# Optimization experiments

Measured on AMD Instinct MI355X. Metric: run time of the kernel, lower is better.

## Reference

```python
import jax, jax.numpy as jnp
import numpy as np

N = 100000
E = 1200000
D_IN, D_HID, D_OUT = 64, 64, 32


def setup_inputs() -> dict:
    key = jax.random.key(0)
    ks = jax.random.split(key, 8)
    x = jax.random.normal(ks[0], (N, D_IN), dtype=jnp.float32)
    edge_index = jax.random.randint(ks[1], (2, E), 0, N, dtype=jnp.int64)
    s_in = 1.0 / np.sqrt(D_IN)
    s_hid = 1.0 / np.sqrt(D_HID)
    return {
        "x": x,
        "edge_index": edge_index,
        "W1_l": jax.random.normal(ks[2], (D_IN, D_HID), dtype=jnp.float32) * s_in,
        "W1_r": jax.random.normal(ks[3], (D_IN, D_HID), dtype=jnp.float32) * s_in,
        "b1": jnp.zeros((D_HID,), dtype=jnp.float32),
        "W2_l": jax.random.normal(ks[4], (D_HID, D_OUT), dtype=jnp.float32) * s_hid,
        "W2_r": jax.random.normal(ks[5], (D_HID, D_OUT), dtype=jnp.float32) * s_hid,
        "b2": jnp.zeros((D_OUT,), dtype=jnp.float32),
    }


def _sage_conv(h, src, dst, W_l, W_r, b, n_nodes):
    # mean aggregation of source features onto destination nodes
    summed = jax.ops.segment_sum(h[src], dst, num_segments=n_nodes)  # [N, d]
    deg = jax.ops.segment_sum(jnp.ones((src.shape[0],), h.dtype), dst,
                              num_segments=n_nodes)  # [N]
    mean = summed / jnp.maximum(deg, 1.0)[:, None]
    # PyG SAGEConv: lin_l(aggr) + lin_r(x); bias lives on lin_l
    return mean @ W_l + b + h @ W_r


def reference(x, edge_index, W1_l, W1_r, b1, W2_l, W2_r, b2):
    src, dst = edge_index[0], edge_index[1]
    n = x.shape[0]
    h = jax.nn.relu(_sage_conv(x, src, dst, W1_l, W1_r, b1, n))
    return _sage_conv(h, src, dst, W2_l, W2_r, b2, n)
```

## Files before the change

kernel.cpp:

```cpp
#include <hip/hip_runtime.h>
#include <hip/hip_bf16.h>


#define D1 64
#define NQ 256
#define SUBN 391
#define QCAP 5632
#define LCAP 11520
#define BE 5120

static __device__ __forceinline__ float bf2f(ushort u) {
    unsigned int x = ((unsigned int)u) << 16;
    return __uint_as_float(x);
}
static __device__ __forceinline__ ushort f2bf(float f) {
    union { __hip_bfloat16 b; ushort u; } cv;
    cv.b = __float2bfloat16(f);
    return cv.u;
}
static __device__ __forceinline__ float lo2f(unsigned u) {
    return __uint_as_float(u << 16);
}
static __device__ __forceinline__ float hi2f(unsigned u) {
    return __uint_as_float(u & 0xffff0000u);
}
static __device__ __forceinline__ unsigned packbf(float x, float y) {
    return (unsigned)f2bf(x) | ((unsigned)f2bf(y) << 16);
}


__global__ __launch_bounds__(256)
void compact_edges256(const int* __restrict__ src, const int* __restrict__ dst,
                      int* __restrict__ tail, int2* __restrict__ queue, int E) {
    __shared__ int hist[NQ];
    __shared__ int base[NQ];
    int tid = threadIdx.x;
    int e0 = blockIdx.x * BE;
    int e1 = min(E, e0 + BE);

    hist[tid] = 0;
    __syncthreads();
    for (int e = e0 + tid; e < e1; e += 256)
        atomicAdd(&hist[dst[e] / SUBN], 1);
    __syncthreads();
    base[tid] = atomicAdd(&tail[tid], hist[tid]);
    hist[tid] = 0;
    __syncthreads();
    for (int e = e0 + tid; e < e1; e += 256) {
        int d = dst[e];
        int s = src[e];
        int p = d / SUBN;
        int pos = base[p] + atomicAdd(&hist[p], 1);
        if (pos < QCAP) queue[(size_t)p * QCAP + pos] = make_int2(s, d);
    }
}


__global__ __launch_bounds__(256)
void csr_build_local(const int2* __restrict__ queue, const int* __restrict__ tail,
                     int2* __restrict__ info, int* __restrict__ nbr, int N) {
    __shared__ int lcnt[512];
    __shared__ int psum[256];
    __shared__ int lnbr[LCAP];
    int tid = threadIdx.x;
    int p = blockIdx.x;
    int lo = p * SUBN;
    int nt = min(tail[p], QCAP);
    const int2* q = queue + (size_t)p * QCAP;
    int gbase = p * LCAP;

    lcnt[tid] = 0; lcnt[tid + 256] = 0;
    __syncthreads();
    for (int e = tid; e < nt; e += 256)
        atomicAdd(&lcnt[q[e].y - lo], 1);
    __syncthreads();

    int d0 = lcnt[2 * tid], d1 = lcnt[2 * tid + 1];
    int p0 = (d0 + 15) & ~15, p1 = (d1 + 15) & ~15;
    int s = p0 + p1;
    psum[tid] = s;
    __syncthreads();
    for (int off = 1; off < 256; off <<= 1) {
        int a = (tid >= off) ? psum[tid - off] : 0;
        __syncthreads();
        psum[tid] += a;
        __syncthreads();
    }
    int st0 = psum[tid] - s;
    int st1 = st0 + p0;
    int ptot = psum[255];

    {
        int li = 2 * tid, n = lo + li;
        if (li < SUBN && n < N) info[n] = make_int2(gbase + st0, d0);
        lcnt[li] = st0;
        li = 2 * tid + 1; n = lo + li;
        if (li < SUBN && n < N) info[n] = make_int2(gbase + st1, d1);
        lcnt[li] = st1;
    }
    __syncthreads();

    for (int e = tid; e < nt; e += 256) {
        int2 pr = q[e];
        int pos = atomicAdd(&lcnt[pr.y - lo], 1);
        lnbr[pos] = pr.x;
    }
    __syncthreads();

    for (int j = st0 + d0; j < st0 + p0; ++j) lnbr[j] = N;
    for (int j = st1 + d1; j < st1 + p1; ++j) lnbr[j] = N;
    __syncthreads();

    for (int i = tid; i < ptot; i += 256)
        nbr[gbase + i] = lnbr[i];
}


__global__ __launch_bounds__(256)
void cvt_bf16_init(const float* __restrict__ in, ushort* __restrict__ xh,
                   ushort* __restrict__ y2, int* __restrict__ tail,
                   int n4, int N) {
    int i = blockIdx.x * 256 + threadIdx.x;
    if (i < n4) {
        float4 v = *(const float4*)&in[(size_t)i * 4];
        ushort4 u;
        u.x = f2bf(v.x); u.y = f2bf(v.y); u.z = f2bf(v.z); u.w = f2bf(v.w);
        *(ushort4*)&xh[(size_t)i * 4] = u;
    }
    if (blockIdx.x == 0) tail[threadIdx.x] = 0;
    if (blockIdx.x == 1) {
        if (threadIdx.x < D1) xh[(size_t)N * D1 + threadIdx.x] = 0;
        if (threadIdx.x < 32) y2[(size_t)N * 32 + threadIdx.x] = 0;
    }
}


#define ACC8(u) do { \
    a0 += lo2f((u).x); a1 += hi2f((u).x); \
    a2 += lo2f((u).y); a3 += hi2f((u).y); \
    a4 += lo2f((u).z); a5 += hi2f((u).z); \
    a6 += lo2f((u).w); a7 += hi2f((u).w); } while (0)

__global__ __launch_bounds__(256)
void gather_mean8(const ushort* __restrict__ feat,
                  const int2* __restrict__ info,
                  const int* __restrict__ nbr,
                  ushort* __restrict__ mean, int N) {
    int wid  = (blockIdx.x * 256 + threadIdx.x) >> 6;
    int lane = threadIdx.x & 63;
    if (wid >= N) return;
    int2 ii = info[wid];
    int deg = ii.y;
    int m8 = (deg + 7) & ~7;
    const int* nb = nbr + ii.x;
    int r = lane >> 3;
    int c = lane & 7;
    const uint4* f4 = (const uint4*)feat;

    float a0 = 0, a1 = 0, a2 = 0, a3 = 0, a4 = 0, a5 = 0, a6 = 0, a7 = 0;
    int i = 0;
    for (; i + 16 <= m8; i += 16) {
        int e0 = nb[i + r];
        int e1 = nb[i + 8 + r];
        uint4 u0 = f4[(size_t)e0 * 8 + c];
        uint4 u1 = f4[(size_t)e1 * 8 + c];
        ACC8(u0);
        ACC8(u1);
    }
    if (i < m8) {
        int e0 = nb[i + r];
        uint4 u0 = f4[(size_t)e0 * 8 + c];
        ACC8(u0);
    }

    a0 += __shfl_xor(a0, 8, 64); a0 += __shfl_xor(a0, 16, 64); a0 += __shfl_xor(a0, 32, 64);
    a1 += __shfl_xor(a1, 8, 64); a1 += __shfl_xor(a1, 16, 64); a1 += __shfl_xor(a1, 32, 64);
    a2 += __shfl_xor(a2, 8, 64); a2 += __shfl_xor(a2, 16, 64); a2 += __shfl_xor(a2, 32, 64);
    a3 += __shfl_xor(a3, 8, 64); a3 += __shfl_xor(a3, 16, 64); a3 += __shfl_xor(a3, 32, 64);
    a4 += __shfl_xor(a4, 8, 64); a4 += __shfl_xor(a4, 16, 64); a4 += __shfl_xor(a4, 32, 64);
    a5 += __shfl_xor(a5, 8, 64); a5 += __shfl_xor(a5, 16, 64); a5 += __shfl_xor(a5, 32, 64);
    a6 += __shfl_xor(a6, 8, 64); a6 += __shfl_xor(a6, 16, 64); a6 += __shfl_xor(a6, 32, 64);
    a7 += __shfl_xor(a7, 8, 64); a7 += __shfl_xor(a7, 16, 64); a7 += __shfl_xor(a7, 32, 64);

    if (r == 0) {
        float inv = 1.0f / fmaxf((float)deg, 1.0f);
        uint4 o;
        o.x = packbf(a0 * inv, a1 * inv);
        o.y = packbf(a2 * inv, a3 * inv);
        o.z = packbf(a4 * inv, a5 * inv);
        o.w = packbf(a6 * inv, a7 * inv);
        ((uint4*)mean)[(size_t)wid * 8 + c] = o;
    }
}


__global__ __launch_bounds__(256)
void gather_mean16(const ushort* __restrict__ feat,
                   const int2* __restrict__ info,
                   const int* __restrict__ nbr,
                   ushort* __restrict__ mean, int N) {
    int wid  = (blockIdx.x * 256 + threadIdx.x) >> 6;
    int lane = threadIdx.x & 63;
    if (wid >= N) return;
    int2 ii = info[wid];
    int deg = ii.y;
    int m16 = (deg + 15) & ~15;
    const int* nb = nbr + ii.x;
    int r = lane >> 2;
    int c = lane & 3;
    const uint4* f4 = (const uint4*)feat;

    float a0 = 0, a1 = 0, a2 = 0, a3 = 0, a4 = 0, a5 = 0, a6 = 0, a7 = 0;
    int i = 0;
    for (; i + 32 <= m16; i += 32) {
        int e0 = nb[i + r];
        int e1 = nb[i + 16 + r];
        uint4 u0 = f4[(size_t)e0 * 4 + c];
        uint4 u1 = f4[(size_t)e1 * 4 + c];
        ACC8(u0);
        ACC8(u1);
    }
    if (i < m16) {
        int e0 = nb[i + r];
        uint4 u0 = f4[(size_t)e0 * 4 + c];
        ACC8(u0);
    }

    a0 += __shfl_xor(a0, 4, 64); a0 += __shfl_xor(a0, 8, 64); a0 += __shfl_xor(a0, 16, 64); a0 += __shfl_xor(a0, 32, 64);
    a1 += __shfl_xor(a1, 4, 64); a1 += __shfl_xor(a1, 8, 64); a1 += __shfl_xor(a1, 16, 64); a1 += __shfl_xor(a1, 32, 64);
    a2 += __shfl_xor(a2, 4, 64); a2 += __shfl_xor(a2, 8, 64); a2 += __shfl_xor(a2, 16, 64); a2 += __shfl_xor(a2, 32, 64);
    a3 += __shfl_xor(a3, 4, 64); a3 += __shfl_xor(a3, 8, 64); a3 += __shfl_xor(a3, 16, 64); a3 += __shfl_xor(a3, 32, 64);
    a4 += __shfl_xor(a4, 4, 64); a4 += __shfl_xor(a4, 8, 64); a4 += __shfl_xor(a4, 16, 64); a4 += __shfl_xor(a4, 32, 64);
    a5 += __shfl_xor(a5, 4, 64); a5 += __shfl_xor(a5, 8, 64); a5 += __shfl_xor(a5, 16, 64); a5 += __shfl_xor(a5, 32, 64);
    a6 += __shfl_xor(a6, 4, 64); a6 += __shfl_xor(a6, 8, 64); a6 += __shfl_xor(a6, 16, 64); a6 += __shfl_xor(a6, 32, 64);
    a7 += __shfl_xor(a7, 4, 64); a7 += __shfl_xor(a7, 8, 64); a7 += __shfl_xor(a7, 16, 64); a7 += __shfl_xor(a7, 32, 64);

    if (r == 0) {
        float inv = 1.0f / fmaxf((float)deg, 1.0f);
        uint4 o;
        o.x = packbf(a0 * inv, a1 * inv);
        o.y = packbf(a2 * inv, a3 * inv);
        o.z = packbf(a4 * inv, a5 * inv);
        o.w = packbf(a6 * inv, a7 * inv);
        ((uint4*)mean)[(size_t)wid * 4 + c] = o;
    }
}


#define TA_STRIDE 66

__global__ __launch_bounds__(256)
void dense_sage1(const ushort* __restrict__ Am,
                 const ushort* __restrict__ Ax,
                 const float* __restrict__ Wm,
                 const float* __restrict__ Wx,
                 const float* __restrict__ bias,
                 const float* __restrict__ W2l,
                 ushort* __restrict__ hh,
                 ushort* __restrict__ y2,
                 int N) {
    __shared__ char smraw[128 * TA_STRIDE * 2];
    ushort* ta = (ushort*)smraw;
    float*  to = (float*)smraw;

    int tid  = threadIdx.x;
    int w    = tid >> 6;
    int lane = tid & 63;
    int n0 = blockIdx.x * 64;

    #pragma unroll
    for (int i = 0; i < 8; ++i) {
        int flat = i * 256 + tid;
        int row  = flat >> 4;
        int c4   = (flat & 15) * 4;
        const ushort* A = (row < 64) ? Am : Ax;
        int node = row & 63;
        int grow = n0 + node;
        ushort4 u = make_ushort4(0, 0, 0, 0);
        if (grow < N) u = *(const ushort4*)&A[(size_t)grow * D1 + c4];
        int kb = ((row < 64) ? 0 : 64) + c4;
        ta[(kb + 0) * TA_STRIDE + node] = u.x;
        ta[(kb + 1) * TA_STRIDE + node] = u.y;
        ta[(kb + 2) * TA_STRIDE + node] = u.z;
        ta[(kb + 3) * TA_STRIDE + node] = u.w;
    }
    __syncthreads();

    int jb = __builtin_amdgcn_readfirstlane(w * 16);
    float c[16];
    #pragma unroll
    for (int j = 0; j < 16; ++j) c[j] = bias[jb + j];

    #pragma unroll 4
    for (int k = 0; k < 64; ++k) {
        float a = bf2f(ta[k * TA_STRIDE + lane]);
        #pragma unroll
        for (int j = 0; j < 16; ++j)
            c[j] = fmaf(a, Wm[k * 64 + jb + j], c[j]);
    }
    #pragma unroll 4
    for (int k = 0; k < 64; ++k) {
        float a = bf2f(ta[(64 + k) * TA_STRIDE + lane]);
        #pragma unroll
        for (int j = 0; j < 16; ++j)
            c[j] = fmaf(a, Wx[k * 64 + jb + j], c[j]);
    }
    #pragma unroll
    for (int j = 0; j < 16; ++j) c[j] = fmaxf(c[j], 0.0f);

    __syncthreads();
    #pragma unroll
    for (int j = 0; j < 16; ++j) to[(jb + j) * 65 + lane] = c[j];
    __syncthreads();

    #pragma unroll
    for (int i = 0; i < 4; ++i) {
        int flat = i * 256 + tid;
        int node = flat >> 4;
        int q    = flat & 15;
        int grow = n0 + node;
        if (grow < N) {
            ushort4 u;
            u.x = f2bf(to[(q * 4 + 0) * 65 + node]);
            u.y = f2bf(to[(q * 4 + 1) * 65 + node]);
            u.z = f2bf(to[(q * 4 + 2) * 65 + node]);
            u.w = f2bf(to[(q * 4 + 3) * 65 + node]);
            *(ushort4*)&hh[(size_t)grow * D1 + q * 4] = u;
        }
    }

    int jb2 = __builtin_amdgcn_readfirstlane(w * 8);
    float c2[8];
    #pragma unroll
    for (int j = 0; j < 8; ++j) c2[j] = 0.0f;
    #pragma unroll 4
    for (int k = 0; k < 64; ++k) {
        float a = to[k * 65 + lane];
        #pragma unroll
        for (int j = 0; j < 8; ++j)
            c2[j] = fmaf(a, W2l[k * 32 + jb2 + j], c2[j]);
    }
    __syncthreads();
    #pragma unroll
    for (int j = 0; j < 8; ++j) to[(jb2 + j) * 65 + lane] = c2[j];
    __syncthreads();

    #pragma unroll
    for (int i = 0; i < 2; ++i) {
        int flat = i * 256 + tid;
        int node = flat >> 3;
        int q    = flat & 7;
        int grow = n0 + node;
        if (grow < N) {
            ushort4 u;
            u.x = f2bf(to[(q * 4 + 0) * 65 + node]);
            u.y = f2bf(to[(q * 4 + 1) * 65 + node]);
            u.z = f2bf(to[(q * 4 + 2) * 65 + node]);
            u.w = f2bf(to[(q * 4 + 3) * 65 + node]);
            *(ushort4*)&y2[(size_t)grow * 32 + q * 4] = u;
        }
    }
}


__global__ __launch_bounds__(256)
void dense_sage2(const ushort* __restrict__ Ax,
                 const ushort* __restrict__ mY2,
                 const float* __restrict__ Wx,
                 const float* __restrict__ bias,
                 float* __restrict__ outp, int N) {
    __shared__ char smraw[64 * TA_STRIDE * 2 + 32 * 65 * 4];
    ushort* ta = (ushort*)smraw;
    float*  to = (float*)(smraw + 64 * TA_STRIDE * 2);

    int tid  = threadIdx.x;
    int w    = tid >> 6;
    int lane = tid & 63;
    int n0 = blockIdx.x * 64;

    #pragma unroll
    for (int i = 0; i < 4; ++i) {
        int flat = i * 256 + tid;
        int row  = flat >> 4;
        int c4   = (flat & 15) * 4;
        int grow = n0 + row;
        ushort4 u = make_ushort4(0, 0, 0, 0);
        if (grow < N) u = *(const ushort4*)&Ax[(size_t)grow * D1 + c4];
        ta[(c4 + 0) * TA_STRIDE + row] = u.x;
        ta[(c4 + 1) * TA_STRIDE + row] = u.y;
        ta[(c4 + 2) * TA_STRIDE + row] = u.z;
        ta[(c4 + 3) * TA_STRIDE + row] = u.w;
    }
    __syncthreads();

    int jb = __builtin_amdgcn_readfirstlane(w * 8);
    float c[8];
    #pragma unroll
    for (int j = 0; j < 8; ++j) c[j] = bias[jb + j];

    #pragma unroll 4
    for (int k = 0; k < 64; ++k) {
        float a = bf2f(ta[k * TA_STRIDE + lane]);
        #pragma unroll
        for (int j = 0; j < 8; ++j)
            c[j] = fmaf(a, Wx[k * 32 + jb + j], c[j]);
    }

    #pragma unroll
    for (int j = 0; j < 8; ++j) to[(jb + j) * 65 + lane] = c[j];
    __syncthreads();

    #pragma unroll
    for (int i = 0; i < 2; ++i) {
        int flat = i * 256 + tid;
        int node = flat >> 3;
        int q    = flat & 7;
        int grow = n0 + node;
        if (grow < N) {
            ushort4 m = *(const ushort4*)&mY2[(size_t)grow * 32 + q * 4];
            float4 v;
            v.x = to[(q * 4 + 0) * 65 + node] + bf2f(m.x);
            v.y = to[(q * 4 + 1) * 65 + node] + bf2f(m.y);
            v.z = to[(q * 4 + 2) * 65 + node] + bf2f(m.z);
            v.w = to[(q * 4 + 3) * 65 + node] + bf2f(m.w);
            *(float4*)&outp[(size_t)grow * 32 + q * 4] = v;
        }
    }
}


extern "C" void kernel_launch(void* const* d_in, const int* in_sizes, int n_in,
                              void* d_out, int out_size, void* d_ws, size_t ws_size,
                              hipStream_t stream) {
    const float* x   = (const float*)d_in[0];
    const int*   ei  = (const int*)d_in[1];
    const float* W1l = (const float*)d_in[2];
    const float* W1r = (const float*)d_in[3];
    const float* b1  = (const float*)d_in[4];
    const float* W2l = (const float*)d_in[5];
    const float* W2r = (const float*)d_in[6];
    const float* b2  = (const float*)d_in[7];
    float* out = (float*)d_out;

    int N = in_sizes[0] / D1;
    int E = in_sizes[1] / 2;
    const int* src = ei;
    const int* dst = ei + E;

    char* ws = (char*)d_ws;
    auto alignup = [](size_t v) { return (v + 255) & ~(size_t)255; };
    size_t off = 0;
    int*    tail  = (int*)(ws + off);    off += alignup(NQ * 4);
    int2*   queue = (int2*)(ws + off);   off += alignup((size_t)NQ * QCAP * 8);
    int*    nbr   = (int*)(ws + off);    off += alignup((size_t)NQ * LCAP * 4);
    int2*   info  = (int2*)(ws + off);   off += alignup((size_t)N * 8);
    ushort* xh    = (ushort*)(ws + off); off += alignup((size_t)(N + 1) * D1 * 2);
    ushort* hh    = (ushort*)(ws + off); off += alignup((size_t)(N + 1) * D1 * 2);
    ushort* y2    = (ushort*)(ws + off); off += alignup((size_t)(N + 1) * 32 * 2);
    ushort* mean1  = (ushort*)d_out;
    ushort* meanY2 = xh;

    int gb = (N + 3) / 4;
    int db = (N + 63) / 64;
    int cb = ((N * D1 / 4) + 255) / 256;
    int ab = (E + BE - 1) / BE;

    cvt_bf16_init<<<cb, 256, 0, stream>>>(x, xh, y2, tail, N * D1 / 4, N);
    compact_edges256<<<ab, 256, 0, stream>>>(src, dst, tail, queue, E);
    csr_build_local<<<NQ, 256, 0, stream>>>(queue, tail, info, nbr, N);

    gather_mean8<<<gb, 256, 0, stream>>>(xh, info, nbr, mean1, N);
    dense_sage1<<<db, 256, 0, stream>>>(mean1, xh, W1l, W1r, b1, W2l, hh, y2, N);
    gather_mean16<<<gb, 256, 0, stream>>>(y2, info, nbr, meanY2, N);
    dense_sage2<<<db, 256, 0, stream>>>(hh, meanY2, W2r, b2, out, N);
}
```

Before: 156.7 us.

## Fuse second-layer root projection into dense_sage1 and finalize output in gather

The first dense kernel now also computes h@W2_r and writes it as fp32, instead of writing h to a bf16 buffer. The second gather kernel adds its mean-aggregated W2_l result, the stored root term and the bias, and writes the final output directly. This removes the dense_sage2 launch and the hh write and re-read. In exchange it writes and reads a 32-wide fp32 root buffer (128 bytes per node instead of hh's 128 bytes in bf16) and adds more FMAs to dense_sage1.

```diff
diff --git a/kernel.cpp b/kernel.cpp
--- a/kernel.cpp
+++ b/kernel.cpp
@@ -118,7 +118,7 @@
 
 __global__ __launch_bounds__(256)
 void cvt_bf16_init(const float* __restrict__ in, ushort* __restrict__ xh,
-                   ushort* __restrict__ y2, int* __restrict__ tail,
+                   ushort* __restrict__ y2l, int* __restrict__ tail,
                    int n4, int N) {
     int i = blockIdx.x * 256 + threadIdx.x;
     if (i < n4) {
@@ -130,7 +130,7 @@
     if (blockIdx.x == 0) tail[threadIdx.x] = 0;
     if (blockIdx.x == 1) {
         if (threadIdx.x < D1) xh[(size_t)N * D1 + threadIdx.x] = 0;
-        if (threadIdx.x < 32) y2[(size_t)N * 32 + threadIdx.x] = 0;
+        if (threadIdx.x < 32) y2l[(size_t)N * 32 + threadIdx.x] = 0;
     }
 }
 
@@ -195,10 +195,12 @@
 
 
 __global__ __launch_bounds__(256)
-void gather_mean16(const ushort* __restrict__ feat,
-                   const int2* __restrict__ info,
-                   const int* __restrict__ nbr,
-                   ushort* __restrict__ mean, int N) {
+void gather_out(const ushort* __restrict__ y2l,
+                const float* __restrict__ y2r,
+                const float* __restrict__ b2,
+                const int2* __restrict__ info,
+                const int* __restrict__ nbr,
+                float* __restrict__ outp, int N) {
     int wid  = (blockIdx.x * 256 + threadIdx.x) >> 6;
     int lane = threadIdx.x & 63;
     if (wid >= N) return;
@@ -208,7 +210,7 @@
     const int* nb = nbr + ii.x;
     int r = lane >> 2;
     int c = lane & 3;
-    const uint4* f4 = (const uint4*)feat;
+    const uint4* f4 = (const uint4*)y2l;
 
     float a0 = 0, a1 = 0, a2 = 0, a3 = 0, a4 = 0, a5 = 0, a6 = 0, a7 = 0;
     int i = 0;
@@ -237,12 +239,20 @@
 
     if (r == 0) {
         float inv = 1.0f / fmaxf((float)deg, 1.0f);
-        uint4 o;
-        o.x = packbf(a0 * inv, a1 * inv);
-        o.y = packbf(a2 * inv, a3 * inv);
-        o.z = packbf(a4 * inv, a5 * inv);
-        o.w = packbf(a6 * inv, a7 * inv);
-        ((uint4*)mean)[(size_t)wid * 4 + c] = o;
+        size_t o = (size_t)wid * 32 + c * 8;
+        float4 r0 = *(const float4*)&y2r[o];
+        float4 r1 = *(const float4*)&y2r[o + 4];
+        float4 v0, v1;
+        v0.x = fmaf(a0, inv, r0.x + b2[c * 8 + 0]);
+        v0.y = fmaf(a1, inv, r0.y + b2[c * 8 + 1]);
+        v0.z = fmaf(a2, inv, r0.z + b2[c * 8 + 2]);
+        v0.w = fmaf(a3, inv, r0.w + b2[c * 8 + 3]);
+        v1.x = fmaf(a4, inv, r1.x + b2[c * 8 + 4]);
+        v1.y = fmaf(a5, inv, r1.y + b2[c * 8 + 5]);
+        v1.z = fmaf(a6, inv, r1.z + b2[c * 8 + 6]);
+        v1.w = fmaf(a7, inv, r1.w + b2[c * 8 + 7]);
+        *(float4*)&outp[o] = v0;
+        *(float4*)&outp[o + 4] = v1;
     }
 }
 
@@ -256,12 +266,15 @@
                  const float* __restrict__ Wx,
                  const float* __restrict__ bias,
                  const float* __restrict__ W2l,
-                 ushort* __restrict__ hh,
-                 ushort* __restrict__ y2,
+                 const float* __restrict__ W2r,
+                 ushort* __restrict__ y2l,
+                 float* __restrict__ y2r,
                  int N) {
     __shared__ char smraw[128 * TA_STRIDE * 2];
     ushort* ta = (ushort*)smraw;
     float*  to = (float*)smraw;
+    float*  tA = (float*)smraw;
+    float*  tB = ((float*)smraw) + 32 * 65;
 
     int tid  = threadIdx.x;
     int w    = tid >> 6;
@@ -313,36 +326,25 @@
     for (int j = 0; j < 16; ++j) to[(jb + j) * 65 + lane] = c[j];
     __syncthreads();
 
-    #pragma unroll
-    for (int i = 0; i < 4; ++i) {
-        int flat = i * 256 + tid;
-        int node = flat >> 4;
-        int q    = flat & 15;
-        int grow = n0 + node;
-        if (grow < N) {
-            ushort4 u;
-            u.x = f2bf(to[(q * 4 + 0) * 65 + node]);
-            u.y = f2bf(to[(q * 4 + 1) * 65 + node]);
-            u.z = f2bf(to[(q * 4 + 2) * 65 + node]);
-            u.w = f2bf(to[(q * 4 + 3) * 65 + node]);
-            *(ushort4*)&hh[(size_t)grow * D1 + q * 4] = u;
-        }
-    }
-
     int jb2 = __builtin_amdgcn_readfirstlane(w * 8);
-    float c2[8];
-    #pragma unroll
-    for (int j = 0; j < 8; ++j) c2[j] = 0.0f;
+    float c2[8], c3[8];
+    #pragma unroll
+    for (int j = 0; j < 8; ++j) { c2[j] = 0.0f; c3[j] = 0.0f; }
     #pragma unroll 4
     for (int k = 0; k < 64; ++k) {
         float a = to[k * 65 + lane];
         #pragma unroll
-        for (int j = 0; j < 8; ++j)
+        for (int j = 0; j < 8; ++j) {
             c2[j] = fmaf(a, W2l[k * 32 + jb2 + j], c2[j]);
-    }
-    __syncthreads();
-    #pragma unroll
-    for (int j = 0; j < 8; ++j) to[(jb2 + j) * 65 + lane] = c2[j];
+            c3[j] = fmaf(a, W2r[k * 32 + jb2 + j], c3[j]);
+        }
+    }
+    __syncthreads();
+    #pragma unroll
+    for (int j = 0; j < 8; ++j) {
+        tA[(jb2 + j) * 65 + lane] = c2[j];
+        tB[(jb2 + j) * 65 + lane] = c3[j];
+    }
     __syncthreads();
 
     #pragma unroll
@@ -353,63 +355,13 @@
         int grow = n0 + node;
         if (grow < N) {
             ushort4 u;
-            u.x = f2bf(to[(q * 4 + 0) * 65 + node]);
-            u.y = f2bf(to[(q * 4 + 1) * 65 + node]);
-            u.z = f2bf(to[(q * 4 + 2) * 65 + node]);
-            u.w = f2bf(to[(q * 4 + 3) * 65 + node]);
-            *(ushort4*)&y2[(size_t)grow * 32 + q * 4] = u;
+            u.x = f2bf(tA[(q * 4 + 0) * 65 + node]);
+            u.y = f2bf(tA[(q * 4 + 1) * 65 + node]);
+            u.z = f2bf(tA[(q * 4 + 2) * 65 + node]);
+            u.w = f2bf(tA[(q * 4 + 3) * 65 + node]);
+            *(ushort4*)&y2l[(size_t)grow * 32 + q * 4] = u;
         }
     }
-}
-
-
-__global__ __launch_bounds__(256)
-void dense_sage2(const ushort* __restrict__ Ax,
-                 const ushort* __restrict__ mY2,
-                 const float* __restrict__ Wx,
-                 const float* __restrict__ bias,
-                 float* __restrict__ outp, int N) {
-    __shared__ char smraw[64 * TA_STRIDE * 2 + 32 * 65 * 4];
-    ushort* ta = (ushort*)smraw;
-    float*  to = (float*)(smraw + 64 * TA_STRIDE * 2);
-
-    int tid  = threadIdx.x;
-    int w    = tid >> 6;
-    int lane = tid & 63;
-    int n0 = blockIdx.x * 64;
-
-    #pragma unroll
-    for (int i = 0; i < 4; ++i) {
-        int flat = i * 256 + tid;
-        int row  = flat >> 4;
-        int c4   = (flat & 15) * 4;
-        int grow = n0 + row;
-        ushort4 u = make_ushort4(0, 0, 0, 0);
-        if (grow < N) u = *(const ushort4*)&Ax[(size_t)grow * D1 + c4];
-        ta[(c4 + 0) * TA_STRIDE + row] = u.x;
-        ta[(c4 + 1) * TA_STRIDE + row] = u.y;
-        ta[(c4 + 2) * TA_STRIDE + row] = u.z;
-        ta[(c4 + 3) * TA_STRIDE + row] = u.w;
-    }
-    __syncthreads();
-
-    int jb = __builtin_amdgcn_readfirstlane(w * 8);
-    float c[8];
-    #pragma unroll
-    for (int j = 0; j < 8; ++j) c[j] = bias[jb + j];
-
-    #pragma unroll 4
-    for (int k = 0; k < 64; ++k) {
-        float a = bf2f(ta[k * TA_STRIDE + lane]);
-        #pragma unroll
-        for (int j = 0; j < 8; ++j)
-            c[j] = fmaf(a, Wx[k * 32 + jb + j], c[j]);
-    }
-
-    #pragma unroll
-    for (int j = 0; j < 8; ++j) to[(jb + j) * 65 + lane] = c[j];
-    __syncthreads();
-
     #pragma unroll
     for (int i = 0; i < 2; ++i) {
         int flat = i * 256 + tid;
@@ -417,13 +369,12 @@
         int q    = flat & 7;
         int grow = n0 + node;
         if (grow < N) {
-            ushort4 m = *(const ushort4*)&mY2[(size_t)grow * 32 + q * 4];
             float4 v;
-            v.x = to[(q * 4 + 0) * 65 + node] + bf2f(m.x);
-            v.y = to[(q * 4 + 1) * 65 + node] + bf2f(m.y);
-            v.z = to[(q * 4 + 2) * 65 + node] + bf2f(m.z);
-            v.w = to[(q * 4 + 3) * 65 + node] + bf2f(m.w);
-            *(float4*)&outp[(size_t)grow * 32 + q * 4] = v;
+            v.x = tB[(q * 4 + 0) * 65 + node];
+            v.y = tB[(q * 4 + 1) * 65 + node];
+            v.z = tB[(q * 4 + 2) * 65 + node];
+            v.w = tB[(q * 4 + 3) * 65 + node];
+            *(float4*)&y2r[(size_t)grow * 32 + q * 4] = v;
         }
     }
 }
@@ -455,22 +406,20 @@
     int*    nbr   = (int*)(ws + off);    off += alignup((size_t)NQ * LCAP * 4);
     int2*   info  = (int2*)(ws + off);   off += alignup((size_t)N * 8);
     ushort* xh    = (ushort*)(ws + off); off += alignup((size_t)(N + 1) * D1 * 2);
-    ushort* hh    = (ushort*)(ws + off); off += alignup((size_t)(N + 1) * D1 * 2);
-    ushort* y2    = (ushort*)(ws + off); off += alignup((size_t)(N + 1) * 32 * 2);
-    ushort* mean1  = (ushort*)d_out;
-    ushort* meanY2 = xh;
+    ushort* y2l   = (ushort*)(ws + off); off += alignup((size_t)(N + 1) * 32 * 2);
+    float*  y2r   = (float*)(ws + off);  off += alignup((size_t)N * 32 * 4);
+    ushort* mean1 = (ushort*)d_out;
 
     int gb = (N + 3) / 4;
     int db = (N + 63) / 64;
     int cb = ((N * D1 / 4) + 255) / 256;
     int ab = (E + BE - 1) / BE;
 
-    cvt_bf16_init<<<cb, 256, 0, stream>>>(x, xh, y2, tail, N * D1 / 4, N);
+    cvt_bf16_init<<<cb, 256, 0, stream>>>(x, xh, y2l, tail, N * D1 / 4, N);
     compact_edges256<<<ab, 256, 0, stream>>>(src, dst, tail, queue, E);
     csr_build_local<<<NQ, 256, 0, stream>>>(queue, tail, info, nbr, N);
 
     gather_mean8<<<gb, 256, 0, stream>>>(xh, info, nbr, mean1, N);
-    dense_sage1<<<db, 256, 0, stream>>>(mean1, xh, W1l, W1r, b1, W2l, hh, y2, N);
-    gather_mean16<<<gb, 256, 0, stream>>>(y2, info, nbr, meanY2, N);
-    dense_sage2<<<db, 256, 0, stream>>>(hh, meanY2, W2r, b2, out, N);
-}
+    dense_sage1<<<db, 256, 0, stream>>>(mean1, xh, W1l, W1r, b1, W2l, W2r, y2l, y2r, N);
+    gather_out<<<gb, 256, 0, stream>>>(y2l, y2r, b2, info, nbr, out, N);
+}
```

Result: no change. 156.7 us (-0.0%).
